# Kernel optimization log

Measured on AMD Instinct MI355X. Metric: run time of the kernel, lower is better.

Reference implementation:

```python
import jax, jax.numpy as jnp
import numpy as np

N, E, D, L = 10000, 160000, 512, 3
NEG_SLOPE = 0.2
LN_EPS = 1e-5


def setup_inputs() -> dict:
    key = jax.random.key(0)
    ks = jax.random.split(key, 16)
    def rn(k, shape, scale=0.02):
        return jax.random.normal(k, shape, dtype=jnp.float32) * scale
    return {
        "x": jax.random.normal(ks[0], (N, D), dtype=jnp.float32),
        "edge_attr": jax.random.normal(ks[1], (E, 2), dtype=jnp.float32),
        "emb_inv_W": rn(ks[2], (D, D)), "emb_inv_b": jnp.zeros((D,), jnp.float32),
        "emb_org_W": rn(ks[3], (D, D)), "emb_org_b": jnp.zeros((D,), jnp.float32),
        "gat_Wl": rn(ks[4], (L, D, D)), "gat_bl": jnp.zeros((L, D), jnp.float32),
        "gat_Wr": rn(ks[5], (L, D, D)), "gat_br": jnp.zeros((L, D), jnp.float32),
        "gat_We": rn(ks[6], (L, 2, D)),
        "gat_att": rn(ks[7], (L, D), 0.1),
        "gat_bias": jnp.zeros((L, D), jnp.float32),
        "ln_g": jnp.ones((L, D), jnp.float32), "ln_b": jnp.zeros((L, D), jnp.float32),
        "lin0_W": rn(ks[8], (2 * D, D)), "lin0_b": jnp.zeros((D,), jnp.float32),
        "lin1_W": rn(ks[9], (2 * D, D)), "lin1_b": jnp.zeros((D,), jnp.float32),
        "edge_index": jax.random.randint(ks[10], (2, E), 0, N, dtype=jnp.int32),
        "n_inv": 4000,
        "n_unknown": 3000,
    }


def _layernorm(x, g, b):
    m = jnp.mean(x, axis=-1, keepdims=True)
    v = jnp.mean((x - m) ** 2, axis=-1, keepdims=True)
    return (x - m) * jax.lax.rsqrt(v + LN_EPS) * g + b


def _gatv2(x, src, dst, edge_attr, Wl, bl, Wr, br, We, att, bias):
    # single-head GATv2: e_ij = att . leaky_relu(Wl x_j + Wr x_i + We e_ij)
    xl = x @ Wl + bl                                  # [N,D] source transform
    xr = x @ Wr + br                                  # [N,D] target transform
    m = xl[src] + xr[dst] + edge_attr @ We            # [E,D]
    s = jax.nn.leaky_relu(m, NEG_SLOPE) @ att         # [E] attention logits
    smax = jax.ops.segment_max(s, dst, num_segments=N)  # per-target max
    a = jnp.exp(s - smax[dst])
    denom = jax.ops.segment_sum(a, dst, num_segments=N)
    alpha = a / jnp.where(denom[dst] > 0, denom[dst], 1.0)  # [E]
    out = jax.ops.segment_sum(alpha[:, None] * xl[src], dst, num_segments=N)
    return out + bias


def _forward(x, edge_attr, emb_inv_W, emb_inv_b, emb_org_W, emb_org_b,
             gat_Wl, gat_bl, gat_Wr, gat_br, gat_We, gat_att, gat_bias,
             ln_g, ln_b, lin0_W, lin0_b, lin1_W, lin1_b,
             edge_index, n_inv, n_unknown):
    src, dst = edge_index[0], edge_index[1]
    x0 = x[:n_inv] @ emb_inv_W + emb_inv_b           # [n_inv, D]
    x1 = x[n_inv:] @ emb_org_W + emb_org_b           # [N-n_inv, D]
    h = jnp.concatenate([x0, x1], axis=0)            # [N, D]
    for k in range(L):
        hc = _gatv2(h, src, dst, edge_attr,
                    gat_Wl[k], gat_bl[k], gat_Wr[k], gat_br[k],
                    gat_We[k], gat_att[k], gat_bias[k])
        h = jax.nn.relu(_layernorm(hc + h, ln_g[k], ln_b[k]))
    y0 = jnp.concatenate([x0, h[:n_inv]], axis=-1) @ lin0_W + lin0_b          # [n_inv, D]
    y1 = jnp.concatenate([x1[-n_unknown:], h[-n_unknown:]], axis=-1) @ lin1_W + lin1_b  # [n_unknown, D]
    return y0 @ y1.T                                  # [n_inv, n_unknown]


def reference(x, edge_attr, emb_inv_W, emb_inv_b, emb_org_W, emb_org_b,
              gat_Wl, gat_bl, gat_Wr, gat_br, gat_We, gat_att, gat_bias,
              ln_g, ln_b, lin0_W, lin0_b, lin1_W, lin1_b,
              edge_index, n_inv, n_unknown):
    return _forward(x, edge_attr, emb_inv_W, emb_inv_b, emb_org_W, emb_org_b,
                    gat_Wl, gat_bl, gat_Wr, gat_br, gat_We, gat_att, gat_bias,
                    ln_g, ln_b, lin0_W, lin0_b, lin1_W, lin1_b,
                    edge_index, n_inv, n_unknown)
```

## Files before the change

### kernel.cpp

```cpp
#include <hip/hip_runtime.h>
#include <cstddef>
#include <cstdint>

namespace {

using u16 = unsigned short;
typedef __attribute__((ext_vector_type(8))) unsigned short u16x8;
typedef __attribute__((ext_vector_type(8))) short bf16x8;
typedef __attribute__((ext_vector_type(4))) float f32x4;

constexpr int kN    = 10000;
constexpr int kE    = 160000;
constexpr int kD    = 512;
constexpr int kNinv = 4000;
constexpr int kNunk = 3000;
constexpr int kND   = kN * kD;
constexpr int kScanBlocks = (kN + 255) / 256;
constexpr float kLnEps = 1e-5f;

__device__ __forceinline__ float bf2f(u16 u) {
  return __uint_as_float((unsigned)u << 16);
}
__device__ __forceinline__ u16 f2bf(float f) {
  unsigned u = __float_as_uint(f);
  return (u16)((u + 0x7FFFu + ((u >> 16) & 1u)) >> 16);
}

__device__ __forceinline__ void gload_lds16(const void* g, void* l) {
  __builtin_amdgcn_global_load_lds(
      (const __attribute__((address_space(1))) void*)(unsigned long long)(uintptr_t)g,
      (__attribute__((address_space(3))) void*)(unsigned)(uintptr_t)l,
      16, 0, 0);
}

struct Job2 {
  const u16* A1; const u16* A2; const u16* BT; const float* bias;
  u16* Cb; int M; int xSplit;
};

template <bool WRITE_F32, bool WRITE_BF16, bool A_F32>
__global__ __launch_bounds__(256) void gemm_bf16(
    const u16* __restrict__ A1, const u16* __restrict__ A2,
    const u16* __restrict__ BT, const float* __restrict__ bias,
    float* __restrict__ Cf, u16* __restrict__ Cb, u16* __restrict__ Cb2,
    int nsplit, int M, int N, int K, int ldc, Job2 j2) {
  __shared__ u16 As[128 * 64];
  __shared__ u16 Bs[128 * 64];
  const int tid  = threadIdx.x;
  const int lane = tid & 63;
  const int wid  = tid >> 6;

  const int nwg = gridDim.x * gridDim.y;
  int wg = blockIdx.x + gridDim.x * blockIdx.y;
  {
    const int xcd = wg & 7, idx = wg >> 3;
    const int q = nwg >> 3, r = nwg & 7;
    wg = (xcd < r ? xcd * (q + 1) : r * (q + 1) + (xcd - r) * q) + idx;
  }
  int bx = wg % gridDim.x;
  const int ny = wg / gridDim.x;

  const u16* jA1 = A1; const u16* jA2 = A2; const u16* jBT = BT;
  const float* jbias = bias; u16* jCb = Cb; int jM = M;
  if (bx >= j2.xSplit) {
    bx -= j2.xSplit;
    jA1 = j2.A1; jA2 = j2.A2; jBT = j2.BT;
    jbias = j2.bias; jCb = j2.Cb; jM = j2.M;
  }
  const int bm = bx * 128;
  const int bn = ny * 128;

  const int wr = (wid >> 1) * 64;
  const int wc = (wid & 1) * 64;

  f32x4 acc[4][4];
#pragma unroll
  for (int m = 0; m < 4; ++m)
#pragma unroll
    for (int n = 0; n < 4; ++n) acc[m][n] = (f32x4){0.f, 0.f, 0.f, 0.f};

  const int srow = lane >> 3;
  const int slot = lane & 7;
  const size_t astride = (jA2 != nullptr) ? 512 : (size_t)K;

  for (int k0 = 0; k0 < K; k0 += 64) {
    const u16* Ap = jA1;
    int kof = k0;
    if (jA2 != nullptr && k0 >= 512) { Ap = jA2; kof = k0 - 512; }
#pragma unroll
    for (int t = 0; t < 4; ++t) {
      const int inst = wid * 4 + t;
      const int row  = inst * 8 + srow;
      const int scol = ((slot ^ (row & 7)) << 4);
      const int ar   = min(bm + row, jM - 1);
      if constexpr (A_F32) {
        const float* srcf = (const float*)Ap + (size_t)ar * astride + kof + (scol >> 1);
        const float4 v0 = *reinterpret_cast<const float4*>(srcf);
        const float4 v1 = *reinterpret_cast<const float4*>(srcf + 4);
        u16x8 pk;
        pk[0] = f2bf(v0.x); pk[1] = f2bf(v0.y); pk[2] = f2bf(v0.z); pk[3] = f2bf(v0.w);
        pk[4] = f2bf(v1.x); pk[5] = f2bf(v1.y); pk[6] = f2bf(v1.z); pk[7] = f2bf(v1.w);
        *reinterpret_cast<u16x8*>((char*)As + inst * 1024 + lane * 16) = pk;
      } else {
        gload_lds16((const char*)Ap + ((size_t)ar * astride + kof) * 2 + scol,
                    (char*)As + inst * 1024);
      }
    }
#pragma unroll
    for (int t = 0; t < 4; ++t) {
      const int inst = wid * 4 + t;
      const int row  = inst * 8 + srow;
      const int scol = ((slot ^ (row & 7)) << 4);
      const int bc   = min(bn + row, N - 1);
      gload_lds16((const char*)jBT + ((size_t)bc * K + k0) * 2 + scol,
                  (char*)Bs + inst * 1024);
    }
    asm volatile("s_waitcnt vmcnt(0)" ::: "memory");
    __syncthreads();

#pragma unroll
    for (int kk = 0; kk < 2; ++kk) {
      bf16x8 af[4], bfr[4];
#pragma unroll
      for (int m = 0; m < 4; ++m) {
        const int r = wr + m * 16 + (lane & 15);
        const int s = kk * 4 + (lane >> 4);
        af[m] = *(const bf16x8*)((const char*)As + r * 128 + ((s ^ (r & 7)) << 4));
      }
#pragma unroll
      for (int n = 0; n < 4; ++n) {
        const int c = wc + n * 16 + (lane & 15);
        const int s = kk * 4 + (lane >> 4);
        bfr[n] = *(const bf16x8*)((const char*)Bs + c * 128 + ((s ^ (c & 7)) << 4));
      }
#pragma unroll
      for (int m = 0; m < 4; ++m)
#pragma unroll
        for (int n = 0; n < 4; ++n)
          acc[m][n] = __builtin_amdgcn_mfma_f32_16x16x32_bf16(bfr[n], af[m],
                                                              acc[m][n], 0, 0, 0);
    }
    __syncthreads();
  }

#pragma unroll
  for (int m = 0; m < 4; ++m) {
    const int r = bm + wr + m * 16 + (lane & 15);
    if (r >= jM) continue;
#pragma unroll
    for (int n = 0; n < 4; ++n) {
      const int c0 = bn + wc + n * 16 + ((lane >> 4) << 2);
      if (c0 >= N) continue;
      float4 bv = make_float4(0.f, 0.f, 0.f, 0.f);
      if (jbias != nullptr) bv = *reinterpret_cast<const float4*>(jbias + c0);
      float v0 = acc[m][n][0] + bv.x;
      float v1 = acc[m][n][1] + bv.y;
      float v2 = acc[m][n][2] + bv.z;
      float v3 = acc[m][n][3] + bv.w;
      if (WRITE_F32) {
        float4 o; o.x = v0; o.y = v1; o.z = v2; o.w = v3;
        *reinterpret_cast<float4*>(Cf + (size_t)r * ldc + c0) = o;
      }
      if (WRITE_BF16) {
        u16* dstp = jCb;
        int c = c0;
        if (Cb2 != nullptr && c0 >= nsplit) { dstp = Cb2; c = c0 - nsplit; }
        ushort4 o;
        o.x = f2bf(v0); o.y = f2bf(v1); o.z = f2bf(v2); o.w = f2bf(v3);
        *reinterpret_cast<ushort4*>(dstp + (size_t)r * ldc + c) = o;
      }
    }
  }
}

__global__ __launch_bounds__(256) void gat_fused_kernel(
    const u16* __restrict__ xl, const u16* __restrict__ xr,
    const int* __restrict__ esrcS, const float2* __restrict__ eaS,
    const int* __restrict__ offs, const float* __restrict__ We,
    const float* __restrict__ att, const float* __restrict__ bias,
    const float* __restrict__ lng, const float* __restrict__ lnb,
    const u16* __restrict__ resid, u16* __restrict__ hb) {
  __shared__ float accLDS[4][512];
  __shared__ float wsLDS[4];
  const int wid = threadIdx.x >> 6, lane = threadIdx.x & 63;
  const int n = blockIdx.x;
  const int d8 = lane * 8;

  float r8[8], w0[8], w1[8], a06[8], a04[8];
  {
    const u16x8 rv = *(const u16x8*)(xr + (size_t)n * kD + d8);
#pragma unroll
    for (int i = 0; i < 8; ++i) {
      r8[i] = bf2f(rv[i]);
      w0[i] = We[d8 + i];
      w1[i] = We[kD + d8 + i];
      const float a = att[d8 + i];
      a06[i] = 0.6f * a;
      a04[i] = 0.4f * a;
    }
  }

  float acc[8];
#pragma unroll
  for (int j = 0; j < 8; ++j) acc[j] = 0.f;
  float l_run = 0.f;

  const int beg = offs[n], end = offs[n + 1];
  const int cnt = end - beg;
  const int q = cnt >> 2, r = cnt & 3;
  const int myCnt = q + ((wid < r) ? 1 : 0);
  const int myBeg = beg + wid * q + min(wid, r);

  int sv = 0;
  float2 e2 = make_float2(0.f, 0.f);
  if (lane < myCnt) {
    sv = esrcS[myBeg + lane];
    e2 = eaS[myBeg + lane];
  }

  for (int i = 0; i < myCnt; i += 4) {
    const int k = myCnt - i;
    u16x8 rows[4];
#pragma unroll
    for (int t = 0; t < 4; ++t)
      if (t < k)
        rows[t] = *(const u16x8*)(xl + (size_t)__shfl(sv, i + t) * kD + d8);
    float s[4];
#pragma unroll
    for (int t = 0; t < 4; ++t) {
      s[t] = 0.f;
      if (t < k) {
        const float ex = __shfl(e2.x, i + t), ey = __shfl(e2.y, i + t);
#pragma unroll
        for (int j = 0; j < 8; ++j) {
          const float m = bf2f(rows[t][j]) + r8[j] + ex * w0[j] + ey * w1[j];
          s[t] += a06[j] * m + a04[j] * fabsf(m);
        }
      }
    }
#pragma unroll
    for (int off = 32; off > 0; off >>= 1)
#pragma unroll
      for (int t = 0; t < 4; ++t)
        if (t < k) s[t] += __shfl_xor(s[t], off);
    float qv[4];
    float ws = 0.f;
#pragma unroll
    for (int t = 0; t < 4; ++t) {
      qv[t] = (t < k) ? __expf(s[t]) : 0.f;
      ws += qv[t];
    }
    l_run += ws;
#pragma unroll
    for (int j = 0; j < 8; ++j) {
      float v = acc[j];
#pragma unroll
      for (int t = 0; t < 4; ++t)
        if (t < k) v += qv[t] * bf2f(rows[t][j]);
      acc[j] = v;
    }
  }

  if (lane == 0) wsLDS[wid] = l_run;
#pragma unroll
  for (int j = 0; j < 8; ++j) accLDS[wid][j * 64 + lane] = acc[j];
  __syncthreads();

  if (wid == 0) {
    const float l = wsLDS[0] + wsLDS[1] + wsLDS[2] + wsLDS[3];
    const float inv = 1.f / (l > 0.f ? l : 1.f);
    float aT[8];
#pragma unroll
    for (int j = 0; j < 8; ++j)
      aT[j] = accLDS[0][j * 64 + lane] + accLDS[1][j * 64 + lane] +
              accLDS[2][j * 64 + lane] + accLDS[3][j * 64 + lane];

    float xv[8];
    float sum = 0.f, sq = 0.f;
    {
      const u16x8 hv8 = *(const u16x8*)(resid + (size_t)n * kD + d8);
#pragma unroll
      for (int j = 0; j < 8; ++j) {
        xv[j] = bf2f(hv8[j]) + aT[j] * inv + bias[d8 + j];
        sum += xv[j];
        sq  += xv[j] * xv[j];
      }
    }
#pragma unroll
    for (int off = 32; off > 0; off >>= 1) {
      sum += __shfl_xor(sum, off);
      sq  += __shfl_xor(sq, off);
    }
    const float mean = sum * (1.f / kD);
    const float var  = sq * (1.f / kD) - mean * mean;
    const float rs = rsqrtf(var + kLnEps);
    u16x8 pk;
#pragma unroll
    for (int j = 0; j < 8; ++j) {
      const float y = fmaxf((xv[j] - mean) * rs * lng[d8 + j] + lnb[d8 + j], 0.f);
      pk[j] = f2bf(y);
    }
    *(u16x8*)(hb + (size_t)n * kD + d8) = pk;
  }
}

struct TxJobs {
  const float* src[10];
  u16* dst[10];
  int K[10];
  const float* bl; const float* br; float* catB;
  int* counts; int* done;
};

__global__ __launch_bounds__(256) void transpose_all_kernel(TxJobs jobs) {
  const int z = blockIdx.z;
  if (z == 10) {
    const int lid = (blockIdx.y * 32 + blockIdx.x) * 256 + threadIdx.x;
    if (lid < 3 * 1024) {
      const int k = lid >> 10, j = lid & 1023;
      jobs.catB[lid] = (j < 512) ? jobs.bl[k * 512 + j] : jobs.br[k * 512 + j - 512];
    }
    const int cid = lid - 3 * 1024;
    if (cid >= 0 && cid < kN) jobs.counts[cid] = 0;
    if (cid == kN) jobs.done[0] = 0;
    return;
  }
  const int K = jobs.K[z];
  const int k0 = blockIdx.x * 32;
  if (k0 >= K) return;
  const int n0 = blockIdx.y * 32;
  const float* W = jobs.src[z];
  u16* WT = jobs.dst[z];
  __shared__ float t[32][33];
  const int lx = threadIdx.x & 31, ly = threadIdx.x >> 5;
#pragma unroll
  for (int r = 0; r < 32; r += 8)
    t[ly + r][lx] = W[(size_t)(k0 + ly + r) * 512 + n0 + lx];
  __syncthreads();
#pragma unroll
  for (int r = 0; r < 32; r += 8)
    WT[(size_t)(n0 + ly + r) * K + k0 + lx] = f2bf(t[lx][ly + r]);
}

__global__ void count_kernel(const int* __restrict__ dst, int* __restrict__ counts) {
  const int e = blockIdx.x * 256 + threadIdx.x;
  if (e < kE) atomicAdd(&counts[dst[e]], 1);
}
__global__ __launch_bounds__(256) void scan_fused_kernel(
    const int* __restrict__ counts, int* __restrict__ offsL,
    int* __restrict__ bsum, int* __restrict__ boff, int* __restrict__ done) {
  __shared__ int buf[256];
  __shared__ int lastFlag;
  const int tid = threadIdx.x, bid = blockIdx.x;
  const int i = bid * 256 + tid;
  const int v = (i < kN) ? counts[i] : 0;
  buf[tid] = v;
  __syncthreads();
  for (int off = 1; off < 256; off <<= 1) {
    const int t = (tid >= off) ? buf[tid - off] : 0;
    __syncthreads();
    buf[tid] += t;
    __syncthreads();
  }
  if (i < kN) offsL[i] = buf[tid] - v;
  if (tid == 255) bsum[bid] = buf[255];
  __syncthreads();
  __threadfence();
  if (tid == 0) lastFlag = (atomicAdd(done, 1) == kScanBlocks - 1);
  __syncthreads();
  if (lastFlag && tid < 64) {
    __threadfence();
    const int b = (tid < kScanBlocks) ? atomicAdd(&bsum[tid], 0) : 0;
    int incl = b;
#pragma unroll
    for (int off = 1; off < 64; off <<= 1) {
      const int t = __shfl_up(incl, off);
      if (tid >= off) incl += t;
    }
    if (tid < kScanBlocks) boff[tid] = incl - b;
  }
}
__global__ __launch_bounds__(256) void scan_add_kernel(
    const int* __restrict__ offsL, const int* __restrict__ boff,
    int* __restrict__ offs, int* __restrict__ pos) {
  const int i = blockIdx.x * 256 + threadIdx.x;
  if (i < kN) {
    const int o = offsL[i] + boff[i >> 8];
    offs[i] = o;
    pos[i] = o;
  }
  if (i == 0) offs[kN] = kE;
}
__global__ void scatter_kernel(const int* __restrict__ dst,
                               const int* __restrict__ src,
                               const float* __restrict__ ea,
                               int* __restrict__ pos,
                               int* __restrict__ esrcS,
                               float2* __restrict__ eaS) {
  const int e = blockIdx.x * 256 + threadIdx.x;
  if (e >= kE) return;
  const int p = atomicAdd(&pos[dst[e]], 1);
  esrcS[p] = src[e];
  eaS[p] = *(const float2*)(ea + (size_t)e * 2);
}

}

extern "C" void kernel_launch(void* const* d_in, const int* in_sizes, int n_in,
                              void* d_out, int out_size, void* d_ws, size_t ws_size,
                              hipStream_t stream) {
  const float* x         = (const float*)d_in[0];
  const float* edge_attr = (const float*)d_in[1];
  const float* emb_inv_W = (const float*)d_in[2];
  const float* emb_inv_b = (const float*)d_in[3];
  const float* emb_org_W = (const float*)d_in[4];
  const float* emb_org_b = (const float*)d_in[5];
  const float* gat_Wl    = (const float*)d_in[6];
  const float* gat_bl    = (const float*)d_in[7];
  const float* gat_Wr    = (const float*)d_in[8];
  const float* gat_br    = (const float*)d_in[9];
  const float* gat_We    = (const float*)d_in[10];
  const float* gat_att   = (const float*)d_in[11];
  const float* gat_bias  = (const float*)d_in[12];
  const float* ln_g      = (const float*)d_in[13];
  const float* ln_b      = (const float*)d_in[14];
  const float* lin0_W    = (const float*)d_in[15];
  const float* lin0_b    = (const float*)d_in[16];
  const float* lin1_W    = (const float*)d_in[17];
  const float* lin1_b    = (const float*)d_in[18];
  const int*   edge_idx  = (const int*)d_in[19];
  const int* src = edge_idx;
  const int* dst = edge_idx + kE;
  float* out = (float*)d_out;

  float* catB = (float*)d_ws;
  u16* hb0  = (u16*)(catB + 3072);
  u16* hb   = hb0 + kND;
  u16* xlB  = hb + kND;
  u16* xrB  = xlB + kND;
  u16* y0b  = xrB + kND;
  u16* y1b  = y0b + kNinv * kD;
  u16* embInvT = y1b + kNunk * kD;
  u16* embOrgT = embInvT + 262144;
  u16* WlrT    = embOrgT + 262144;
  u16* lin0T   = WlrT + 3 * 524288;
  u16* lin1T   = lin0T + 524288;
  int* counts  = (int*)(lin1T + 524288);
  int* offsL   = counts + kN;
  int* offs    = offsL + kN;
  int* pos     = offs + kN + 1;
  int* bsum    = pos + kN;
  int* boff    = bsum + kScanBlocks;
  int* done    = boff + kScanBlocks;
  int* esrcS   = done + 1;
  float2* eaS  = (float2*)(esrcS + kE);

  const dim3 blk(256);
  auto cdiv = [](int a, int b) { return (a + b - 1) / b; };
  Job2 jNone{};
  jNone.xSplit = 0x7FFFFFFF;

  {
    TxJobs j;
    j.src[0] = emb_inv_W;  j.dst[0] = embInvT;  j.K[0] = 512;
    j.src[1] = emb_org_W;  j.dst[1] = embOrgT;  j.K[1] = 512;
    for (int k = 0; k < 3; ++k) {
      j.src[2 + k] = gat_Wl + (size_t)k * kD * kD;
      j.dst[2 + k] = WlrT + (size_t)k * 524288;
      j.K[2 + k] = 512;
      j.src[5 + k] = gat_Wr + (size_t)k * kD * kD;
      j.dst[5 + k] = WlrT + (size_t)k * 524288 + 262144;
      j.K[5 + k] = 512;
    }
    j.src[8] = lin0_W; j.dst[8] = lin0T; j.K[8] = 1024;
    j.src[9] = lin1_W; j.dst[9] = lin1T; j.K[9] = 1024;
    j.bl = gat_bl; j.br = gat_br; j.catB = catB;
    j.counts = counts; j.done = done;
    transpose_all_kernel<<<dim3(32, 16, 11), blk, 0, stream>>>(j);
  }

  {
    Job2 je;
    je.A1 = (const u16*)(x + (size_t)kNinv * kD);
    je.A2 = nullptr;
    je.BT = embOrgT;
    je.bias = emb_org_b;
    je.Cb = hb0 + (size_t)kNinv * kD;
    je.M = kN - kNinv;
    je.xSplit = cdiv(kNinv, 128);
    const int gx = je.xSplit + cdiv(kN - kNinv, 128);
    gemm_bf16<false, true, true><<<dim3(gx, 4), blk, 0, stream>>>(
        (const u16*)x, nullptr, embInvT, emb_inv_b, nullptr, hb0, nullptr, 0,
        kNinv, kD, kD, kD, je);
  }

  count_kernel<<<dim3(cdiv(kE, 256)), blk, 0, stream>>>(dst, counts);
  scan_fused_kernel<<<dim3(kScanBlocks), blk, 0, stream>>>(counts, offsL, bsum,
                                                           boff, done);
  scan_add_kernel<<<dim3(kScanBlocks), blk, 0, stream>>>(offsL, boff, offs, pos);
  scatter_kernel<<<dim3(cdiv(kE, 256)), blk, 0, stream>>>(dst, src, edge_attr, pos,
                                                          esrcS, eaS);

  for (int k = 0; k < 3; ++k) {
    const u16* hIn = (k == 0) ? hb0 : hb;
    gemm_bf16<false, true, false><<<dim3(cdiv(kN, 128), 8), blk, 0, stream>>>(
        hIn, nullptr, WlrT + (size_t)k * 524288, catB + k * 1024,
        nullptr, xlB, xrB, 512, kN, 1024, kD, kD, jNone);
    gat_fused_kernel<<<dim3(kN), blk, 0, stream>>>(
        xlB, xrB, esrcS, eaS, offs,
        gat_We + (size_t)k * 2 * kD, gat_att + (size_t)k * kD,
        gat_bias + (size_t)k * kD, ln_g + (size_t)k * kD,
        ln_b + (size_t)k * kD, hIn, hb);
  }

  {
    const size_t off = (size_t)(kN - kNunk) * kD;
    Job2 jh;
    jh.A1 = hb0 + off;
    jh.A2 = hb + off;
    jh.BT = lin1T;
    jh.bias = lin1_b;
    jh.Cb = y1b;
    jh.M = kNunk;
    jh.xSplit = cdiv(kNinv, 128);
    const int gx = jh.xSplit + cdiv(kNunk, 128);
    gemm_bf16<false, true, false><<<dim3(gx, 4), blk, 0, stream>>>(
        hb0, hb, lin0T, lin0_b, nullptr, y0b, nullptr, 0,
        kNinv, kD, 2 * kD, kD, jh);
  }

  gemm_bf16<true, false, false><<<dim3(cdiv(kNinv, 128), cdiv(kNunk, 128)), blk, 0,
                                  stream>>>(
      y0b, nullptr, y1b, nullptr, out, nullptr, nullptr, 0,
      kNinv, kNunk, kD, kNunk, jNone);
}
```

Measured before the change: 360.0 us.

## Fold CSR build into GEMM launches and merge scan kernels

Edge-count atomics now run in an extra grid row of the embedding GEMM, and the edge scatter runs in an extra grid row of the first layer's Wl/Wr GEMM. The scan-add step moves into the last block of the fused scan kernel, which keeps the block offsets in shared memory. Together this removes three small kernel launches and overlaps the irregular atomic work with GEMM tiles. The cost is extra blocks in the GEMM grids and a serial pass over all nodes by a single block at the end of the scan.

```diff
diff --git a/kernel.cpp b/kernel.cpp
--- a/kernel.cpp
+++ b/kernel.cpp
@@ -38,12 +38,18 @@
   u16* Cb; int M; int xSplit;
 };
 
+struct Extra {
+  int mode;
+  const int* dst; const int* src; const float* ea;
+  int* counts; int* pos; int* esrcS; float2* eaS;
+};
+
 template <bool WRITE_F32, bool WRITE_BF16, bool A_F32>
 __global__ __launch_bounds__(256) void gemm_bf16(
     const u16* __restrict__ A1, const u16* __restrict__ A2,
     const u16* __restrict__ BT, const float* __restrict__ bias,
     float* __restrict__ Cf, u16* __restrict__ Cb, u16* __restrict__ Cb2,
-    int nsplit, int M, int N, int K, int ldc, Job2 j2) {
+    int nsplit, int M, int N, int K, int ldc, Job2 j2, Extra ex) {
   __shared__ u16 As[128 * 64];
   __shared__ u16 Bs[128 * 64];
   const int tid  = threadIdx.x;
@@ -59,6 +65,21 @@
   }
   int bx = wg % gridDim.x;
   const int ny = wg / gridDim.x;
+
+  if (ex.mode != 0 && ny == (int)gridDim.y - 1) {
+    const int base = bx * 256 + tid;
+    const int stride = gridDim.x * 256;
+    if (ex.mode == 1) {
+      for (int e = base; e < kE; e += stride) atomicAdd(&ex.counts[ex.dst[e]], 1);
+    } else {
+      for (int e = base; e < kE; e += stride) {
+        const int p = atomicAdd(&ex.pos[ex.dst[e]], 1);
+        ex.esrcS[p] = ex.src[e];
+        ex.eaS[p] = *(const float2*)(ex.ea + (size_t)e * 2);
+      }
+    }
+    return;
+  }
 
   const u16* jA1 = A1; const u16* jA2 = A2; const u16* jBT = BT;
   const float* jbias = bias; u16* jCb = Cb; int jM = M;
@@ -342,14 +363,12 @@
     WT[(size_t)(n0 + ly + r) * K + k0 + lx] = f2bf(t[lx][ly + r]);
 }
 
-__global__ void count_kernel(const int* __restrict__ dst, int* __restrict__ counts) {
-  const int e = blockIdx.x * 256 + threadIdx.x;
-  if (e < kE) atomicAdd(&counts[dst[e]], 1);
-}
 __global__ __launch_bounds__(256) void scan_fused_kernel(
-    const int* __restrict__ counts, int* __restrict__ offsL,
-    int* __restrict__ bsum, int* __restrict__ boff, int* __restrict__ done) {
+    int* __restrict__ counts, int* __restrict__ offsL,
+    int* __restrict__ bsum, int* __restrict__ done,
+    int* __restrict__ offs, int* __restrict__ pos) {
   __shared__ int buf[256];
+  __shared__ int boffS[kScanBlocks];
   __shared__ int lastFlag;
   const int tid = threadIdx.x, bid = blockIdx.x;
   const int i = bid * 256 + tid;
@@ -368,8 +387,9 @@
   __threadfence();
   if (tid == 0) lastFlag = (atomicAdd(done, 1) == kScanBlocks - 1);
   __syncthreads();
-  if (lastFlag && tid < 64) {
-    __threadfence();
+  if (!lastFlag) return;
+  __threadfence();
+  if (tid < 64) {
     const int b = (tid < kScanBlocks) ? atomicAdd(&bsum[tid], 0) : 0;
     int incl = b;
 #pragma unroll
@@ -377,31 +397,15 @@
       const int t = __shfl_up(incl, off);
       if (tid >= off) incl += t;
     }
-    if (tid < kScanBlocks) boff[tid] = incl - b;
-  }
-}
-__global__ __launch_bounds__(256) void scan_add_kernel(
-    const int* __restrict__ offsL, const int* __restrict__ boff,
-    int* __restrict__ offs, int* __restrict__ pos) {
-  const int i = blockIdx.x * 256 + threadIdx.x;
-  if (i < kN) {
-    const int o = offsL[i] + boff[i >> 8];
-    offs[i] = o;
-    pos[i] = o;
-  }
-  if (i == 0) offs[kN] = kE;
-}
-__global__ void scatter_kernel(const int* __restrict__ dst,
-                               const int* __restrict__ src,
-                               const float* __restrict__ ea,
-                               int* __restrict__ pos,
-                               int* __restrict__ esrcS,
-                               float2* __restrict__ eaS) {
-  const int e = blockIdx.x * 256 + threadIdx.x;
-  if (e >= kE) return;
-  const int p = atomicAdd(&pos[dst[e]], 1);
-  esrcS[p] = src[e];
-  eaS[p] = *(const float2*)(ea + (size_t)e * 2);
+    if (tid < kScanBlocks) boffS[tid] = incl - b;
+  }
+  __syncthreads();
+  for (int j = tid; j < kN; j += 256) {
+    const int o = atomicAdd(&offsL[j], 0) + boffS[j >> 8];
+    offs[j] = o;
+    pos[j] = o;
+  }
+  if (tid == 0) offs[kN] = kE;
 }
 
 }
@@ -450,8 +454,7 @@
   int* offs    = offsL + kN;
   int* pos     = offs + kN + 1;
   int* bsum    = pos + kN;
-  int* boff    = bsum + kScanBlocks;
-  int* done    = boff + kScanBlocks;
+  int* done    = bsum + kScanBlocks;
   int* esrcS   = done + 1;
   float2* eaS  = (float2*)(esrcS + kE);
 
@@ -459,6 +462,8 @@
   auto cdiv = [](int a, int b) { return (a + b - 1) / b; };
   Job2 jNone{};
   jNone.xSplit = 0x7FFFFFFF;
+  Extra exNone{};
+  exNone.mode = 0;
 
   {
     TxJobs j;
@@ -488,24 +493,29 @@
     je.Cb = hb0 + (size_t)kNinv * kD;
     je.M = kN - kNinv;
     je.xSplit = cdiv(kNinv, 128);
+    Extra ec{};
+    ec.mode = 1; ec.dst = dst; ec.counts = counts;
     const int gx = je.xSplit + cdiv(kN - kNinv, 128);
-    gemm_bf16<false, true, true><<<dim3(gx, 4), blk, 0, stream>>>(
+    gemm_bf16<false, true, true><<<dim3(gx, 5), blk, 0, stream>>>(
         (const u16*)x, nullptr, embInvT, emb_inv_b, nullptr, hb0, nullptr, 0,
-        kNinv, kD, kD, kD, je);
-  }
-
-  count_kernel<<<dim3(cdiv(kE, 256)), blk, 0, stream>>>(dst, counts);
+        kNinv, kD, kD, kD, je, ec);
+  }
+
   scan_fused_kernel<<<dim3(kScanBlocks), blk, 0, stream>>>(counts, offsL, bsum,
-                                                           boff, done);
-  scan_add_kernel<<<dim3(kScanBlocks), blk, 0, stream>>>(offsL, boff, offs, pos);
-  scatter_kernel<<<dim3(cdiv(kE, 256)), blk, 0, stream>>>(dst, src, edge_attr, pos,
-                                                          esrcS, eaS);
+                                                           done, offs, pos);
 
   for (int k = 0; k < 3; ++k) {
     const u16* hIn = (k == 0) ? hb0 : hb;
-    gemm_bf16<false, true, false><<<dim3(cdiv(kN, 128), 8), blk, 0, stream>>>(
+    Extra ex = exNone;
+    int gy = 8;
+    if (k == 0) {
+      ex.mode = 2; ex.dst = dst; ex.src = src; ex.ea = edge_attr;
+      ex.pos = pos; ex.esrcS = esrcS; ex.eaS = eaS;
+      gy = 9;
+    }
+    gemm_bf16<false, true, false><<<dim3(cdiv(kN, 128), gy), blk, 0, stream>>>(
         hIn, nullptr, WlrT + (size_t)k * 524288, catB + k * 1024,
-        nullptr, xlB, xrB, 512, kN, 1024, kD, kD, jNone);
+        nullptr, xlB, xrB, 512, kN, 1024, kD, kD, jNone, ex);
     gat_fused_kernel<<<dim3(kN), blk, 0, stream>>>(
         xlB, xrB, esrcS, eaS, offs,
         gat_We + (size_t)k * 2 * kD, gat_att + (size_t)k * kD,
@@ -526,11 +536,11 @@
     const int gx = jh.xSplit + cdiv(kNunk, 128);
     gemm_bf16<false, true, false><<<dim3(gx, 4), blk, 0, stream>>>(
         hb0, hb, lin0T, lin0_b, nullptr, y0b, nullptr, 0,
-        kNinv, kD, 2 * kD, kD, jh);
+        kNinv, kD, 2 * kD, kD, jh, exNone);
   }
 
   gemm_bf16<true, false, false><<<dim3(cdiv(kNinv, 128), cdiv(kNunk, 128)), blk, 0,
                                   stream>>>(
       y0b, nullptr, y1b, nullptr, out, nullptr, nullptr, 0,
-      kNinv, kNunk, kD, kNunk, jNone);
-}
+      kNinv, kNunk, kD, kNunk, jNone, exNone);
+}
```

Result: no change. 358.3 us (-0.5%).
